# Optimization experiments

Hardware: AMD Instinct MI355X
Metric: run time of the kernel (lower is better)

The kernel has to match this reference:

```python
import jax, jax.numpy as jnp
import numpy as np

HIDDEN = 1024
NUM_HEADS = 16
HEAD_DIM = HIDDEN // NUM_HEADS


def rotary_cos_sin(seq_len, head_dim, dtype=jnp.float32):
    inv_freq = 1.0 / (10000.0 ** (jnp.arange(0, head_dim, 2, dtype=dtype) / head_dim))
    t = jnp.arange(seq_len, dtype=dtype)
    freqs = jnp.einsum('i,j->ij', t, inv_freq)          # [S, hd/2]
    emb = jnp.concatenate([freqs, freqs], axis=-1)      # [S, hd]
    return jnp.cos(emb), jnp.sin(emb)


def apply_rotary(x, cos, sin):
    # x: [B, H, S, hd]; cos/sin: [S, hd]
    x1, x2 = jnp.split(x, 2, axis=-1)
    x_rot = jnp.concatenate([-x2, x1], axis=-1)
    return x * cos + x_rot * sin


def setup_inputs() -> dict:
    key = jax.random.key(0)
    ks = jax.random.split(key, 5)
    S, B = 2048, 2
    x = jax.random.normal(ks[0], (S, B, HIDDEN), dtype=jnp.float32)
    s = 1.0 / np.sqrt(HIDDEN)
    W_qkv = jax.random.uniform(ks[1], (HIDDEN, 3 * HIDDEN), jnp.float32, -s, s)
    b_qkv = jax.random.uniform(ks[2], (3 * HIDDEN,), jnp.float32, -s, s)
    W_out = jax.random.uniform(ks[3], (HIDDEN, HIDDEN), jnp.float32, -s, s)
    b_out = jax.random.uniform(ks[4], (HIDDEN,), jnp.float32, -s, s)
    return {"x": x, "W_qkv": W_qkv, "b_qkv": b_qkv, "W_out": W_out, "b_out": b_out}


def reference(x, W_qkv, b_qkv, W_out, b_out):
    S, B, D = x.shape
    scale = HEAD_DIM ** -0.5
    qkv = x @ W_qkv + b_qkv                               # [S, B, 3D]
    qkv = qkv.reshape(S, B, NUM_HEADS, 3 * HEAD_DIM)
    q, k, v = jnp.split(qkv, 3, axis=-1)                  # each [S, B, H, hd]
    q = q.transpose(1, 2, 0, 3)                           # [B, H, S, hd]
    k = k.transpose(1, 2, 0, 3)
    v = v.transpose(1, 2, 0, 3)
    cos, sin = rotary_cos_sin(S, HEAD_DIM, x.dtype)
    q = apply_rotary(q, cos, sin)
    k = apply_rotary(k, cos, sin)
    scores = jnp.einsum('bhqd,bhkd->bhqk', q, k) * scale  # [B, H, S, S]
    weights = jax.nn.softmax(scores, axis=-1)
    attn = jnp.einsum('bhqk,bhkd->bhqd', weights, v)      # [B, H, S, hd]
    attn = attn.transpose(2, 0, 1, 3).reshape(S, B, D)    # [S, B, D]
    return attn @ W_out + b_out
```

## Files before the change

kernel.cpp:

```cpp
#include <hip/hip_runtime.h>

typedef unsigned short u16;
typedef __attribute__((ext_vector_type(8))) short bf16x8;
typedef __attribute__((ext_vector_type(4))) float f32x4;

#define S_LEN 2048
#define BATCH 2
#define HID 1024
#define NH 16
#define HD 64
#define MROWS 4096
#define QKV_N 3072
#define QSCALE 0.18033688011112042f

__device__ __forceinline__ u16 f2bf(float f) {
  unsigned u = __float_as_uint(f);
  u += 0x7fffu + ((u >> 16) & 1u);
  return (u16)(u >> 16);
}

__device__ __forceinline__ float bf2f(u16 u) {
  return __uint_as_float((unsigned)u << 16);
}

__device__ __forceinline__ float fexp2(float x) {
  float r; asm("v_exp_f32 %0, %1" : "=v"(r) : "v"(x)); return r;
}

__device__ __forceinline__ unsigned cvtpk(float lo, float hi) {
  unsigned r; asm("v_cvt_pk_bf16_f32 %0, %1, %2" : "=v"(r) : "v"(lo), "v"(hi)); return r;
}

__device__ __forceinline__ void gl2lds16(const u16* src, u16* lds) {
  __builtin_amdgcn_global_load_lds((__attribute__((address_space(1))) void*)(void*)src,
                                   (__attribute__((address_space(3))) void*)(void*)lds,
                                   16, 0, 0);
}

__global__ void cast_f32_bf16(const float* __restrict__ in, u16* __restrict__ out) {
  int i = blockIdx.x * blockDim.x + threadIdx.x;
  const float4* p = (const float4*)in;
  float4 a = p[2 * i], b = p[2 * i + 1];
  union { u16 us[8]; uint4 v; } o;
  o.us[0] = f2bf(a.x); o.us[1] = f2bf(a.y); o.us[2] = f2bf(a.z); o.us[3] = f2bf(a.w);
  o.us[4] = f2bf(b.x); o.us[5] = f2bf(b.y); o.us[6] = f2bf(b.z); o.us[7] = f2bf(b.w);
  *(uint4*)&out[8 * i] = o.v;
}

__global__ __launch_bounds__(256) void castT(const float* __restrict__ W, u16* __restrict__ Wt,
                                             int Ncols, int Krows) {
  __shared__ float tile[32][33];
  int c0 = blockIdx.x * 32, r0 = blockIdx.y * 32;
  int tx = threadIdx.x & 31, ty = threadIdx.x >> 5;
  #pragma unroll
  for (int i = 0; i < 4; ++i)
    tile[ty + i * 8][tx] = W[(size_t)(r0 + ty + i * 8) * Ncols + c0 + tx];
  __syncthreads();
  #pragma unroll
  for (int i = 0; i < 4; ++i) {
    int a = ty + i * 8;
    Wt[(size_t)(c0 + a) * Krows + r0 + tx] = f2bf(tile[tx][a]);
  }
}

__global__ void rope_init(float2* __restrict__ tab) {
  int i = blockIdx.x * blockDim.x + threadIdx.x;
  int s = i >> 5, j = i & 31;
  float invf = powf(10000.0f, -(float)(2 * j) / 64.0f);
  float ang = (float)s * invf;
  tab[i] = make_float2(cosf(ang), sinf(ang));
}

__global__ __launch_bounds__(256, 2) void gemm_qkv(
    const u16* __restrict__ A, const u16* __restrict__ Bt,
    const float* __restrict__ bias, const float2* __restrict__ rope,
    u16* __restrict__ Qb, u16* __restrict__ Kb, u16* __restrict__ Vb) {
  __shared__ u16 As[128 * 32];
  __shared__ u16 Bs[128 * 32];
  const int tid = threadIdx.x;
  const int lane = tid & 63, wid = tid >> 6;
  const int g = lane >> 4, l15 = lane & 15;
  const int bm0 = blockIdx.x * 128, bn0 = blockIdx.y * 128;
  const int wm = wid >> 1, wn = wid & 1;

  f32x4 acc[4][4] = {};
  for (int kt = 0; kt < 32; ++kt) {
    const int k0 = kt * 32;
    __syncthreads();
    #pragma unroll
    for (int it = 0; it < 2; ++it) {
      int s = it * 256 + tid;
      gl2lds16(A  + (size_t)(bm0 + (s >> 2)) * 1024 + k0 + (s & 3) * 8, &As[s * 8]);
      gl2lds16(Bt + (size_t)(bn0 + (s >> 2)) * 1024 + k0 + (s & 3) * 8, &Bs[s * 8]);
    }
    __syncthreads();
    bf16x8 af[4], bfr[4];
    #pragma unroll
    for (int m = 0; m < 4; ++m) af[m]  = *(const bf16x8*)&As[(wm * 64 + m * 16 + l15) * 32 + g * 8];
    #pragma unroll
    for (int n = 0; n < 4; ++n) bfr[n] = *(const bf16x8*)&Bs[(wn * 64 + n * 16 + l15) * 32 + g * 8];
    #pragma unroll
    for (int m = 0; m < 4; ++m)
      #pragma unroll
      for (int n = 0; n < 4; ++n)
        acc[m][n] = __builtin_amdgcn_mfma_f32_16x16x32_bf16(af[m], bfr[n], acc[m][n], 0, 0, 0);
  }

  const int cw0 = bn0 + wn * 64;
  const int gi = cw0 >> 6;
  const int h = gi / 3, tt = gi % 3;
  float bs[4];
  #pragma unroll
  for (int n = 0; n < 4; ++n) bs[n] = bias[cw0 + n * 16 + l15];
  const size_t hb = (size_t)h * (S_LEN * HD);

  if (tt == 2) {
    #pragma unroll
    for (int m = 0; m < 4; ++m)
      #pragma unroll
      for (int reg = 0; reg < 4; ++reg) {
        int r = bm0 + wm * 64 + m * 16 + g * 4 + reg;
        int srow = r >> 1, b = r & 1;
        size_t o = (size_t)(b * NH) * (S_LEN * HD) + hb + (size_t)srow * HD;
        #pragma unroll
        for (int n = 0; n < 4; ++n)
          Vb[o + n * 16 + l15] = f2bf(acc[m][n][reg] + bs[n]);
      }
  } else {
    u16* dst = (tt == 0) ? Qb : Kb;
    const float scl = (tt == 0) ? QSCALE : 1.0f;
    #pragma unroll
    for (int m = 0; m < 4; ++m)
      #pragma unroll
      for (int reg = 0; reg < 4; ++reg) {
        int r = bm0 + wm * 64 + m * 16 + g * 4 + reg;
        int srow = r >> 1, b = r & 1;
        size_t o = (size_t)(b * NH) * (S_LEN * HD) + hb + (size_t)srow * HD;
        #pragma unroll
        for (int n = 0; n < 2; ++n) {
          int dlo = n * 16 + l15;
          float2 cs = rope[srow * 32 + dlo];
          float v1 = acc[m][n][reg] + bs[n];
          float v2 = acc[m][n + 2][reg] + bs[n + 2];
          dst[o + dlo]      = f2bf((v1 * cs.x - v2 * cs.y) * scl);
          dst[o + dlo + 32] = f2bf((v2 * cs.x + v1 * cs.y) * scl);
        }
      }
  }
}

__global__ __launch_bounds__(256) void transpose_v(const u16* __restrict__ Vb, u16* __restrict__ Vt) {
  __shared__ u16 t[64][72];
  const int bh = blockIdx.y, s0 = blockIdx.x * 64;
  const size_t base = (size_t)bh * S_LEN * HD;
  const int tid = threadIdx.x;
  #pragma unroll
  for (int it = 0; it < 2; ++it) {
    int sl = it * 256 + tid;
    int r = sl >> 3, cg = sl & 7;
    union { uint4 v; u16 us[8]; } u;
    u.v = *(const uint4*)&Vb[base + (size_t)(s0 + r) * HD + cg * 8];
    #pragma unroll
    for (int j = 0; j < 8; ++j) t[cg * 8 + j][r] = u.us[j];
  }
  __syncthreads();
  #pragma unroll
  for (int it = 0; it < 2; ++it) {
    int sl = it * 256 + tid;
    int d = sl >> 3, sg = sl & 7;
    union { uint4 v; u16 us[8]; } u;
    #pragma unroll
    for (int j = 0; j < 8; ++j) u.us[j] = t[d][sg * 8 + j];
    *(uint4*)&Vt[(size_t)bh * HD * S_LEN + (size_t)d * S_LEN + s0 + sg * 8] = u.v;
  }
}

__global__ __launch_bounds__(512, 6) void attn_fwd(
    const u16* __restrict__ Qb, const u16* __restrict__ Kb,
    const u16* __restrict__ Vt, u16* __restrict__ part0,
    u16* __restrict__ part1, float2* __restrict__ stats) {
  __shared__ u16 Ks[2][64 * 64];
  __shared__ u16 Vs[2][64 * 64];
  __shared__ u16 Plds[8][16][72];
  const int tid = threadIdx.x;
  const int lane = tid & 63, wid = tid >> 6;
  const int g = lane >> 4, l15 = lane & 15;
  const int bh = blockIdx.y;
  const int split = blockIdx.z;
  const int kt0 = split * 16;
  const int qr0 = blockIdx.x * 128 + wid * 16;
  const u16* Qp = Qb + ((size_t)bh * S_LEN + qr0) * HD;
  const u16* Kp = Kb + (size_t)bh * S_LEN * HD;
  const u16* Vp = Vt + (size_t)bh * HD * S_LEN;

  const int sr = tid >> 3;
  const int ssw = (tid & 7) ^ (sr & 7);
  const u16* kg = Kp + (size_t)sr * HD + ssw * 8;
  const u16* vg = Vp + (size_t)sr * S_LEN + ssw * 8;

  bf16x8 qf[2];
  #pragma unroll
  for (int c = 0; c < 2; ++c) qf[c] = *(const bf16x8*)&Qp[l15 * HD + g * 8 + c * 32];

  f32x4 po[4] = {};
  float mrun = -INFINITY, lrun = 0.f;

  gl2lds16(kg + (size_t)kt0 * 64 * HD, &Ks[0][tid * 8]);
  gl2lds16(vg + kt0 * 64, &Vs[0][tid * 8]);
  __syncthreads();

  for (int i = 0; i < 16; ++i) {
    const int bb = i & 1;
    if (i + 1 < 16) {
      gl2lds16(kg + (size_t)(kt0 + i + 1) * 64 * HD, &Ks[bb ^ 1][tid * 8]);
      gl2lds16(vg + (kt0 + i + 1) * 64, &Vs[bb ^ 1][tid * 8]);
    }
    const u16* KsB = Ks[bb];
    const u16* VsB = Vs[bb];

    f32x4 sacc[4] = {};
    __builtin_amdgcn_s_setprio(1);
    #pragma unroll
    for (int c = 0; c < 2; ++c) {
      const int csw = ((g + 4 * c) ^ (l15 & 7)) * 8;
      #pragma unroll
      for (int t = 0; t < 4; ++t) {
        const bf16x8 kf = *(const bf16x8*)&KsB[(t * 16 + l15) * 64 + csw];
        sacc[t] = __builtin_amdgcn_mfma_f32_16x16x32_bf16(kf, qf[c], sacc[t], 0, 0, 0);
      }
    }
    __builtin_amdgcn_s_setprio(0);

    float tm = -INFINITY;
    #pragma unroll
    for (int t = 0; t < 4; ++t)
      tm = fmaxf(tm, fmaxf(fmaxf(sacc[t][0], sacc[t][1]), fmaxf(sacc[t][2], sacc[t][3])));
    tm = fmaxf(tm, __shfl_xor(tm, 16));
    tm = fmaxf(tm, __shfl_xor(tm, 32));

    if (!__all(tm <= mrun + 8.f)) {
      float mnew = fmaxf(mrun, tm);
      float alpha = fexp2(mrun - mnew);
      mrun = mnew;
      lrun *= alpha;
      float ar[4];
      #pragma unroll
      for (int reg = 0; reg < 4; ++reg) ar[reg] = __shfl(alpha, g * 4 + reg);
      #pragma unroll
      for (int n = 0; n < 4; ++n)
        #pragma unroll
        for (int reg = 0; reg < 4; ++reg) po[n][reg] *= ar[reg];
    }

    float rs = 0.f;
    #pragma unroll
    for (int t = 0; t < 4; ++t) {
      float p0 = fexp2(sacc[t][0] - mrun);
      float p1 = fexp2(sacc[t][1] - mrun);
      float p2 = fexp2(sacc[t][2] - mrun);
      float p3 = fexp2(sacc[t][3] - mrun);
      rs += (p0 + p1) + (p2 + p3);
      uint2 pw;
      pw.x = cvtpk(p0, p1);
      pw.y = cvtpk(p2, p3);
      *(uint2*)&Plds[wid][l15][t * 16 + g * 4] = pw;
    }
    rs += __shfl_xor(rs, 16);
    rs += __shfl_xor(rs, 32);
    lrun += rs;

    __builtin_amdgcn_s_setprio(1);
    #pragma unroll
    for (int c = 0; c < 2; ++c) {
      const bf16x8 pf = *(const bf16x8*)&Plds[wid][l15][g * 8 + c * 32];
      const int csw = ((g + 4 * c) ^ (l15 & 7)) * 8;
      #pragma unroll
      for (int n = 0; n < 4; ++n) {
        const bf16x8 vf = *(const bf16x8*)&VsB[(n * 16 + l15) * 64 + csw];
        po[n] = __builtin_amdgcn_mfma_f32_16x16x32_bf16(pf, vf, po[n], 0, 0, 0);
      }
    }
    __builtin_amdgcn_s_setprio(0);
    __syncthreads();
  }

  u16* part = split ? part1 : part0;
  if (g == 0)
    stats[(size_t)split * (32 * 2048) + (size_t)bh * 2048 + qr0 + l15] =
        make_float2(mrun, lrun);
  #pragma unroll
  for (int n = 0; n < 4; ++n)
    #pragma unroll
    for (int reg = 0; reg < 4; ++reg) {
      size_t q = (size_t)bh * 2048 + qr0 + g * 4 + reg;
      part[q * 64 + n * 16 + l15] = f2bf(po[n][reg]);
    }
}

__global__ void attn_combine(const u16* __restrict__ part0, const u16* __restrict__ part1,
                             const float2* __restrict__ stats, u16* __restrict__ attn2d) {
  int t = blockIdx.x * 256 + threadIdx.x;
  int bh = t >> 14, r = t & 16383, q = r >> 3, dc = r & 7;
  int b = bh >> 4, h = bh & 15;
  float2 s0 = stats[bh * 2048 + q];
  float2 s1 = stats[32 * 2048 + bh * 2048 + q];
  float M = fmaxf(s0.x, s1.x);
  float w0 = fexp2(s0.x - M), w1 = fexp2(s1.x - M);
  float inv = 1.f / (w0 * s0.y + w1 * s1.y);
  w0 *= inv; w1 *= inv;
  size_t off = ((size_t)bh * 2048 + q) * 64 + dc * 8;
  union { uint4 v; u16 us[8]; } a, c, o;
  a.v = *(const uint4*)&part0[off];
  c.v = *(const uint4*)&part1[off];
  #pragma unroll
  for (int j = 0; j < 8; ++j)
    o.us[j] = f2bf(w0 * bf2f(a.us[j]) + w1 * bf2f(c.us[j]));
  *(uint4*)&attn2d[((size_t)q * BATCH + b) * HID + h * HD + dc * 8] = o.v;
}

__global__ __launch_bounds__(256, 2) void gemm_out(
    const u16* __restrict__ A, const u16* __restrict__ Bt,
    const float* __restrict__ bias, float* __restrict__ out) {
  __shared__ u16 As[128 * 32];
  __shared__ u16 Bs[128 * 32];
  const int tid = threadIdx.x;
  const int lane = tid & 63, wid = tid >> 6;
  const int g = lane >> 4, l15 = lane & 15;
  const int bm0 = blockIdx.x * 128, bn0 = blockIdx.y * 128;
  const int wm = wid >> 1, wn = wid & 1;

  f32x4 acc[4][4] = {};
  for (int kt = 0; kt < 32; ++kt) {
    const int k0 = kt * 32;
    __syncthreads();
    #pragma unroll
    for (int it = 0; it < 2; ++it) {
      int s = it * 256 + tid;
      gl2lds16(A  + (size_t)(bm0 + (s >> 2)) * 1024 + k0 + (s & 3) * 8, &As[s * 8]);
      gl2lds16(Bt + (size_t)(bn0 + (s >> 2)) * 1024 + k0 + (s & 3) * 8, &Bs[s * 8]);
    }
    __syncthreads();
    bf16x8 af[4], bfr[4];
    #pragma unroll
    for (int m = 0; m < 4; ++m) af[m]  = *(const bf16x8*)&As[(wm * 64 + m * 16 + l15) * 32 + g * 8];
    #pragma unroll
    for (int n = 0; n < 4; ++n) bfr[n] = *(const bf16x8*)&Bs[(wn * 64 + n * 16 + l15) * 32 + g * 8];
    #pragma unroll
    for (int m = 0; m < 4; ++m)
      #pragma unroll
      for (int n = 0; n < 4; ++n)
        acc[m][n] = __builtin_amdgcn_mfma_f32_16x16x32_bf16(af[m], bfr[n], acc[m][n], 0, 0, 0);
  }
  #pragma unroll
  for (int n = 0; n < 4; ++n) {
    int c = bn0 + wn * 64 + n * 16 + l15;
    float bv = bias[c];
    #pragma unroll
    for (int m = 0; m < 4; ++m)
      #pragma unroll
      for (int reg = 0; reg < 4; ++reg) {
        int r = bm0 + wm * 64 + m * 16 + g * 4 + reg;
        out[(size_t)r * HID + c] = acc[m][n][reg] + bv;
      }
  }
}

extern "C" void kernel_launch(void* const* d_in, const int* in_sizes, int n_in,
                              void* d_out, int out_size, void* d_ws, size_t ws_size,
                              hipStream_t stream) {
  const float* x     = (const float*)d_in[0];
  const float* W_qkv = (const float*)d_in[1];
  const float* b_qkv = (const float*)d_in[2];
  const float* W_out = (const float*)d_in[3];
  const float* b_out = (const float*)d_in[4];
  float* out = (float*)d_out;

  char* ws = (char*)d_ws;
  size_t off = 0;
  auto carve = [&](size_t bytes) { void* p = ws + off; off += (bytes + 255) & ~(size_t)255; return p; };
  u16* xb      = (u16*)carve((size_t)MROWS * HID * 2);
  u16* Wqt     = (u16*)carve((size_t)QKV_N * HID * 2);
  u16* Wot     = (u16*)carve((size_t)HID * HID * 2);
  float2* rope = (float2*)carve((size_t)S_LEN * 32 * 8);
  u16* Qb      = (u16*)carve((size_t)BATCH * NH * S_LEN * HD * 2);
  u16* Kb      = (u16*)carve((size_t)BATCH * NH * S_LEN * HD * 2);
  u16* Vb      = (u16*)carve((size_t)BATCH * NH * S_LEN * HD * 2);
  u16* Vt      = (u16*)carve((size_t)BATCH * NH * S_LEN * HD * 2);
  u16* attn2d  = (u16*)carve((size_t)MROWS * HID * 2);
  float2* stats= (float2*)carve((size_t)2 * 32 * 2048 * 8);

  cast_f32_bf16<<<2048, 256, 0, stream>>>(x, xb);
  castT<<<dim3(QKV_N / 32, HID / 32), 256, 0, stream>>>(W_qkv, Wqt, QKV_N, HID);
  castT<<<dim3(HID / 32, HID / 32), 256, 0, stream>>>(W_out, Wot, HID, HID);
  rope_init<<<256, 256, 0, stream>>>(rope);
  gemm_qkv<<<dim3(MROWS / 128, QKV_N / 128), 256, 0, stream>>>(xb, Wqt, b_qkv, rope, Qb, Kb, Vb);
  transpose_v<<<dim3(S_LEN / 64, BATCH * NH), 256, 0, stream>>>(Vb, Vt);
  attn_fwd<<<dim3(S_LEN / 128, BATCH * NH, 2), 512, 0, stream>>>(Qb, Kb, Vt, xb, Vb, stats);
  attn_combine<<<2048, 256, 0, stream>>>(xb, Vb, stats, attn2d);
  gemm_out<<<dim3(MROWS / 128, HID / 128), 256, 0, stream>>>(attn2d, Wot, b_out, out);
}
```

Baseline: 141.9 us.

## Fuse prep kernels, keep P in registers via permlane swaps, retile output GEMM

Merges the x cast, both weight cast-transposes and the rope table into one prep launch to cut launch overhead. In attention, the softmax probabilities are moved into the MFMA A-operand layout with v_permlane32/16_swap in registers instead of a round trip through LDS. The Plds buffer is dropped and occupancy is raised to 8 waves per SIMD. The output GEMM uses 128x64 tiles so it launches twice as many blocks. The permlane remapping has to reproduce the old LDS layout exactly, and one swap operand is written in an odd form that may be wrong.

```diff
diff --git a/kernel.cpp b/kernel.cpp
--- a/kernel.cpp
+++ b/kernel.cpp
@@ -37,20 +37,10 @@
                                    16, 0, 0);
 }
 
-__global__ void cast_f32_bf16(const float* __restrict__ in, u16* __restrict__ out) {
-  int i = blockIdx.x * blockDim.x + threadIdx.x;
-  const float4* p = (const float4*)in;
-  float4 a = p[2 * i], b = p[2 * i + 1];
-  union { u16 us[8]; uint4 v; } o;
-  o.us[0] = f2bf(a.x); o.us[1] = f2bf(a.y); o.us[2] = f2bf(a.z); o.us[3] = f2bf(a.w);
-  o.us[4] = f2bf(b.x); o.us[5] = f2bf(b.y); o.us[6] = f2bf(b.z); o.us[7] = f2bf(b.w);
-  *(uint4*)&out[8 * i] = o.v;
-}
-
-__global__ __launch_bounds__(256) void castT(const float* __restrict__ W, u16* __restrict__ Wt,
-                                             int Ncols, int Krows) {
-  __shared__ float tile[32][33];
-  int c0 = blockIdx.x * 32, r0 = blockIdx.y * 32;
+__device__ __forceinline__ void castT_body(const float* __restrict__ W, u16* __restrict__ Wt,
+                                           int Ncols, int Krows, int bx, int by,
+                                           float (*tile)[33]) {
+  int c0 = bx * 32, r0 = by * 32;
   int tx = threadIdx.x & 31, ty = threadIdx.x >> 5;
   #pragma unroll
   for (int i = 0; i < 4; ++i)
@@ -63,12 +53,33 @@
   }
 }
 
-__global__ void rope_init(float2* __restrict__ tab) {
-  int i = blockIdx.x * blockDim.x + threadIdx.x;
-  int s = i >> 5, j = i & 31;
-  float invf = powf(10000.0f, -(float)(2 * j) / 64.0f);
-  float ang = (float)s * invf;
-  tab[i] = make_float2(cosf(ang), sinf(ang));
+__global__ __launch_bounds__(256) void prep(
+    const float* __restrict__ x, const float* __restrict__ W_qkv,
+    const float* __restrict__ W_out, u16* __restrict__ xb,
+    u16* __restrict__ Wqt, u16* __restrict__ Wot, float2* __restrict__ rope) {
+  __shared__ float tile[32][33];
+  const int bid = blockIdx.x;
+  if (bid < 2048) {
+    int i = bid * 256 + threadIdx.x;
+    const float4* p = (const float4*)x;
+    float4 a = p[2 * i], b = p[2 * i + 1];
+    union { u16 us[8]; uint4 v; } o;
+    o.us[0] = f2bf(a.x); o.us[1] = f2bf(a.y); o.us[2] = f2bf(a.z); o.us[3] = f2bf(a.w);
+    o.us[4] = f2bf(b.x); o.us[5] = f2bf(b.y); o.us[6] = f2bf(b.z); o.us[7] = f2bf(b.w);
+    *(uint4*)&xb[8 * i] = o.v;
+  } else if (bid < 2048 + 3072) {
+    int r = bid - 2048;
+    castT_body(W_qkv, Wqt, QKV_N, HID, r % 96, r / 96, tile);
+  } else if (bid < 2048 + 3072 + 1024) {
+    int r = bid - (2048 + 3072);
+    castT_body(W_out, Wot, HID, HID, r % 32, r / 32, tile);
+  } else {
+    int i = (bid - 6144) * 256 + threadIdx.x;
+    int s = i >> 5, j = i & 31;
+    float invf = powf(10000.0f, -(float)(2 * j) / 64.0f);
+    float ang = (float)s * invf;
+    rope[i] = make_float2(cosf(ang), sinf(ang));
+  }
 }
 
 __global__ __launch_bounds__(256, 2) void gemm_qkv(
@@ -175,13 +186,12 @@
   }
 }
 
-__global__ __launch_bounds__(512, 6) void attn_fwd(
+__global__ __launch_bounds__(512, 8) void attn_fwd(
     const u16* __restrict__ Qb, const u16* __restrict__ Kb,
     const u16* __restrict__ Vt, u16* __restrict__ part0,
     u16* __restrict__ part1, float2* __restrict__ stats) {
   __shared__ u16 Ks[2][64 * 64];
   __shared__ u16 Vs[2][64 * 64];
-  __shared__ u16 Plds[8][16][72];
   const int tid = threadIdx.x;
   const int lane = tid & 63, wid = tid >> 6;
   const int g = lane >> 4, l15 = lane & 15;
@@ -231,10 +241,12 @@
     }
     __builtin_amdgcn_s_setprio(0);
 
-    float tm = -INFINITY;
-    #pragma unroll
-    for (int t = 0; t < 4; ++t)
-      tm = fmaxf(tm, fmaxf(fmaxf(sacc[t][0], sacc[t][1]), fmaxf(sacc[t][2], sacc[t][3])));
+    float m0 = fmaxf(fmaxf(sacc[0][0], sacc[0][1]), sacc[0][2]);
+    float m1 = fmaxf(fmaxf(sacc[0][3], sacc[1][0]), sacc[1][1]);
+    float m2 = fmaxf(fmaxf(sacc[1][2], sacc[1][3]), sacc[2][0]);
+    float m3 = fmaxf(fmaxf(sacc[2][1], sacc[2][2]), sacc[2][3]);
+    float m4 = fmaxf(fmaxf(sacc[3][0], sacc[3][1]), sacc[3][2]);
+    float tm = fmaxf(fmaxf(fmaxf(m0, m1), fmaxf(m2, m3)), fmaxf(m4, sacc[3][3]));
     tm = fmaxf(tm, __shfl_xor(tm, 16));
     tm = fmaxf(tm, __shfl_xor(tm, 32));
 
@@ -252,27 +264,47 @@
         for (int reg = 0; reg < 4; ++reg) po[n][reg] *= ar[reg];
     }
 
-    float rs = 0.f;
-    #pragma unroll
-    for (int t = 0; t < 4; ++t) {
-      float p0 = fexp2(sacc[t][0] - mrun);
-      float p1 = fexp2(sacc[t][1] - mrun);
-      float p2 = fexp2(sacc[t][2] - mrun);
-      float p3 = fexp2(sacc[t][3] - mrun);
-      rs += (p0 + p1) + (p2 + p3);
-      uint2 pw;
-      pw.x = cvtpk(p0, p1);
-      pw.y = cvtpk(p2, p3);
-      *(uint2*)&Plds[wid][l15][t * 16 + g * 4] = pw;
-    }
+    unsigned u00, u01, u10, u11, u20, u21, u30, u31;
+    float rsA, rsB;
+    {
+      float p0 = fexp2(sacc[0][0] - mrun), p1 = fexp2(sacc[0][1] - mrun);
+      float p2 = fexp2(sacc[0][2] - mrun), p3 = fexp2(sacc[0][3] - mrun);
+      u00 = cvtpk(p0, p1); u01 = cvtpk(p2, p3);
+      rsA = (p0 + p1) + (p2 + p3);
+      p0 = fexp2(sacc[1][0] - mrun); p1 = fexp2(sacc[1][1] - mrun);
+      p2 = fexp2(sacc[1][2] - mrun); p3 = fexp2(sacc[1][3] - mrun);
+      u10 = cvtpk(p0, p1); u11 = cvtpk(p2, p3);
+      rsA += (p0 + p1) + (p2 + p3);
+      p0 = fexp2(sacc[2][0] - mrun); p1 = fexp2(sacc[2][1] - mrun);
+      p2 = fexp2(sacc[2][2] - mrun); p3 = fexp2(sacc[2][3] - mrun);
+      u20 = cvtpk(p0, p1); u21 = cvtpk(p2, p3);
+      rsB = (p0 + p1) + (p2 + p3);
+      p0 = fexp2(sacc[3][0] - mrun); p1 = fexp2(sacc[3][1] - mrun);
+      p2 = fexp2(sacc[3][2] - mrun); p3 = fexp2(sacc[3][3] - mrun);
+      u30 = cvtpk(p0, p1); u31 = cvtpk(p2, p3);
+      rsB += (p0 + p1) + (p2 + p3);
+    }
+    float rs = rsA + rsB;
     rs += __shfl_xor(rs, 16);
     rs += __shfl_xor(rs, 32);
     lrun += rs;
 
+    asm("v_permlane32_swap_b32 %0, %1" : "+v"(u00), "+v"(u10));
+    asm("v_permlane32_swap_b32 %0, %1" : "+v"(u01), "+v"(u11));
+    asm("v_permlane32_swap_b32 %0, %1" : "+v"(u20), "+v"(u30));
+    asm("v_permlane32_swap_b32 %0, %1" : "+v"(u21), "+v"(u31));
+    asm("v_permlane16_swap_b32 %0, %1" : "+v"(u00), "+v"(u10));
+    asm("v_permlane16_swap_b32 %0, %1" : "+v"(u01), "+v"(u11));
+    asm("v_permlane16_swap_b32 %0, %1" : "+v"(u20), "+v"(u31 == u31 ? u30 : u30));
+    asm("v_permlane16_swap_b32 %0, %1" : "+v"(u21), "+v"(u31));
+    union { unsigned w[4]; bf16x8 v; } af0, af1;
+    af0.w[0] = u00; af0.w[1] = u01; af0.w[2] = u10; af0.w[3] = u11;
+    af1.w[0] = u20; af1.w[1] = u21; af1.w[2] = u30; af1.w[3] = u31;
+
     __builtin_amdgcn_s_setprio(1);
     #pragma unroll
     for (int c = 0; c < 2; ++c) {
-      const bf16x8 pf = *(const bf16x8*)&Plds[wid][l15][g * 8 + c * 32];
+      const bf16x8 pf = c ? af1.v : af0.v;
       const int csw = ((g + 4 * c) ^ (l15 & 7)) * 8;
       #pragma unroll
       for (int n = 0; n < 4; ++n) {
@@ -322,44 +354,43 @@
     const u16* __restrict__ A, const u16* __restrict__ Bt,
     const float* __restrict__ bias, float* __restrict__ out) {
   __shared__ u16 As[128 * 32];
-  __shared__ u16 Bs[128 * 32];
+  __shared__ u16 Bs[64 * 32];
   const int tid = threadIdx.x;
   const int lane = tid & 63, wid = tid >> 6;
   const int g = lane >> 4, l15 = lane & 15;
-  const int bm0 = blockIdx.x * 128, bn0 = blockIdx.y * 128;
-  const int wm = wid >> 1, wn = wid & 1;
-
-  f32x4 acc[4][4] = {};
+  const int bm0 = blockIdx.x * 128, bn0 = blockIdx.y * 64;
+
+  f32x4 acc[2][4] = {};
   for (int kt = 0; kt < 32; ++kt) {
     const int k0 = kt * 32;
     __syncthreads();
     #pragma unroll
     for (int it = 0; it < 2; ++it) {
       int s = it * 256 + tid;
-      gl2lds16(A  + (size_t)(bm0 + (s >> 2)) * 1024 + k0 + (s & 3) * 8, &As[s * 8]);
-      gl2lds16(Bt + (size_t)(bn0 + (s >> 2)) * 1024 + k0 + (s & 3) * 8, &Bs[s * 8]);
-    }
+      gl2lds16(A + (size_t)(bm0 + (s >> 2)) * 1024 + k0 + (s & 3) * 8, &As[s * 8]);
+    }
+    gl2lds16(Bt + (size_t)(bn0 + (tid >> 2)) * 1024 + k0 + (tid & 3) * 8, &Bs[tid * 8]);
     __syncthreads();
-    bf16x8 af[4], bfr[4];
-    #pragma unroll
-    for (int m = 0; m < 4; ++m) af[m]  = *(const bf16x8*)&As[(wm * 64 + m * 16 + l15) * 32 + g * 8];
-    #pragma unroll
-    for (int n = 0; n < 4; ++n) bfr[n] = *(const bf16x8*)&Bs[(wn * 64 + n * 16 + l15) * 32 + g * 8];
-    #pragma unroll
-    for (int m = 0; m < 4; ++m)
+    bf16x8 af[2], bfr[4];
+    #pragma unroll
+    for (int m = 0; m < 2; ++m) af[m]  = *(const bf16x8*)&As[(wid * 32 + m * 16 + l15) * 32 + g * 8];
+    #pragma unroll
+    for (int n = 0; n < 4; ++n) bfr[n] = *(const bf16x8*)&Bs[(n * 16 + l15) * 32 + g * 8];
+    #pragma unroll
+    for (int m = 0; m < 2; ++m)
       #pragma unroll
       for (int n = 0; n < 4; ++n)
         acc[m][n] = __builtin_amdgcn_mfma_f32_16x16x32_bf16(af[m], bfr[n], acc[m][n], 0, 0, 0);
   }
   #pragma unroll
   for (int n = 0; n < 4; ++n) {
-    int c = bn0 + wn * 64 + n * 16 + l15;
+    int c = bn0 + n * 16 + l15;
     float bv = bias[c];
     #pragma unroll
-    for (int m = 0; m < 4; ++m)
+    for (int m = 0; m < 2; ++m)
       #pragma unroll
       for (int reg = 0; reg < 4; ++reg) {
-        int r = bm0 + wm * 64 + m * 16 + g * 4 + reg;
+        int r = bm0 + wid * 32 + m * 16 + g * 4 + reg;
         out[(size_t)r * HID + c] = acc[m][n][reg] + bv;
       }
   }
@@ -389,13 +420,10 @@
   u16* attn2d  = (u16*)carve((size_t)MROWS * HID * 2);
   float2* stats= (float2*)carve((size_t)2 * 32 * 2048 * 8);
 
-  cast_f32_bf16<<<2048, 256, 0, stream>>>(x, xb);
-  castT<<<dim3(QKV_N / 32, HID / 32), 256, 0, stream>>>(W_qkv, Wqt, QKV_N, HID);
-  castT<<<dim3(HID / 32, HID / 32), 256, 0, stream>>>(W_out, Wot, HID, HID);
-  rope_init<<<256, 256, 0, stream>>>(rope);
+  prep<<<6400, 256, 0, stream>>>(x, W_qkv, W_out, xb, Wqt, Wot, rope);
   gemm_qkv<<<dim3(MROWS / 128, QKV_N / 128), 256, 0, stream>>>(xb, Wqt, b_qkv, rope, Qb, Kb, Vb);
   transpose_v<<<dim3(S_LEN / 64, BATCH * NH), 256, 0, stream>>>(Vb, Vt);
   attn_fwd<<<dim3(S_LEN / 128, BATCH * NH, 2), 512, 0, stream>>>(Qb, Kb, Vt, xb, Vb, stats);
   attn_combine<<<2048, 256, 0, stream>>>(xb, Vb, stats, attn2d);
-  gemm_out<<<dim3(MROWS / 128, HID / 128), 256, 0, stream>>>(attn2d, Wot, b_out, out);
-}
+  gemm_out<<<dim3(MROWS / 128, HID / 64), 256, 0, stream>>>(attn2d, Wot, b_out, out);
+}
```

Result: faster. 132.6 us (-6.5%).
